# Optimization experiments

Hardware: AMD Instinct MI355X
Metric: run time of the kernel (lower is better)

Reference implementation:

```python
import jax, jax.numpy as jnp
import numpy as np

K = 5            # n_neighbors
N_CLASSES = 100  # number of label classes
EPS = 1e-12


def setup_inputs() -> dict:
    key = jax.random.key(0)
    k1, k2, k3 = jax.random.split(key, 3)
    x = jax.random.normal(k1, (4096, 512), dtype=jnp.float32)
    train_data = jax.random.normal(k2, (100000, 512), dtype=jnp.float32)
    train_labels = jax.random.randint(k3, (100000,), 0, N_CLASSES, dtype=jnp.int32)
    return {"x": x, "train_data": train_data, "train_labels": train_labels}


def reference(x, train_data, train_labels):
    # Pairwise L2 distances: [N_test, N_train]
    x_sq = jnp.sum(x * x, axis=1, keepdims=True)            # [N_test, 1]
    t_sq = jnp.sum(train_data * train_data, axis=1)         # [N_train]
    cross = x @ train_data.T                                 # [N_test, N_train]
    dist = jnp.sqrt(jnp.clip(x_sq + t_sq[None, :] - 2.0 * cross, EPS, None))
    # k smallest distances -> top_k on negated distances
    _, idx = jax.lax.top_k(-dist, K)                          # idx: [N_test, K]
    neighbor_labels = train_labels[idx]                       # [N_test, K]
    # torch.mode picks the most frequent label, smallest value on ties;
    # argmax over per-class counts returns the lowest index on ties -> same semantics.
    counts = jnp.sum(jax.nn.one_hot(neighbor_labels, N_CLASSES, dtype=jnp.int32), axis=1)  # [N_test, C]
    predictions = jnp.argmax(counts, axis=1).astype(jnp.int32)  # [N_test]
    return predictions
```

## Files before the change

kernel.cpp:

```cpp
#include <hip/hip_runtime.h>


#define N_TEST   4096
#define N_TRAIN  100000
#define NT256    391
#define NPAD     100096
#define DIM      512
#define KNN      5
#define NCH      16
#define TD6      6
#define TD8      8
#define PH       17
#define SLAB     16384
#define INF      3.402823466e38f
#define IMAX     0x7fffffff

typedef __attribute__((ext_vector_type(8))) _Float16 f16x8;
typedef __attribute__((ext_vector_type(4))) _Float16 f16x4;
typedef __attribute__((ext_vector_type(4))) float    f32x4;

#define WS_WSI   0u
#define WS_TSQ   2097152u
#define WS_AIMG  2500608u
#define WS_BIMG  111405056u
#define WS_NEED  115861504u

__device__ __forceinline__ void gload_lds16(const void* g, void* l) {
    __builtin_amdgcn_global_load_lds(
        (const __attribute__((address_space(1))) void*)g,
        (__attribute__((address_space(3))) void*)l, 16, 0, 0);
}

__device__ __forceinline__ bool bet(float d, int t, float dd, int tt) {
    return (d < dd) || (d == dd && t < tt);
}

__device__ __forceinline__ void ins6lex(float (&td)[TD6], int (&ti)[TD6], float d, int tg) {
    if (bet(d, tg, td[TD6 - 1], ti[TD6 - 1])) {
        td[TD6 - 1] = d; ti[TD6 - 1] = tg;
        #pragma unroll
        for (int j = TD6 - 1; j > 0; --j) {
            if (bet(td[j], ti[j], td[j - 1], ti[j - 1])) {
                float t0 = td[j]; td[j] = td[j - 1]; td[j - 1] = t0;
                int   i0 = ti[j]; ti[j] = ti[j - 1]; ti[j - 1] = i0;
            }
        }
    }
}

__device__ __forceinline__ void ins8(float (&td)[TD8], int (&ti)[TD8], float d, int tg) {
    if (d < td[TD8 - 1]) {
        td[TD8 - 1] = d; ti[TD8 - 1] = tg;
        #pragma unroll
        for (int j = TD8 - 1; j > 0; --j) {
            if (td[j] < td[j - 1]) {
                float t0 = td[j]; td[j] = td[j - 1]; td[j - 1] = t0;
                int   i0 = ti[j]; ti[j] = ti[j - 1]; ti[j - 1] = i0;
            }
        }
    }
}

__device__ __forceinline__ void ins8lex(float (&td)[TD8], int (&ti)[TD8], float d, int tg) {
    if (bet(d, tg, td[TD8 - 1], ti[TD8 - 1])) {
        td[TD8 - 1] = d; ti[TD8 - 1] = tg;
        #pragma unroll
        for (int j = TD8 - 1; j > 0; --j) {
            if (bet(td[j], ti[j], td[j - 1], ti[j - 1])) {
                float t0 = td[j]; td[j] = td[j - 1]; td[j - 1] = t0;
                int   i0 = ti[j]; ti[j] = ti[j - 1]; ti[j - 1] = i0;
            }
        }
    }
}

__device__ __forceinline__ void ins5lex(float (&td)[KNN], int (&ti)[KNN], float d, int tg) {
    if (bet(d, tg, td[4], ti[4])) {
        if (bet(d, tg, td[3], ti[3])) {
            td[4] = td[3]; ti[4] = ti[3];
            if (bet(d, tg, td[2], ti[2])) {
                td[3] = td[2]; ti[3] = ti[2];
                if (bet(d, tg, td[1], ti[1])) {
                    td[2] = td[1]; ti[2] = ti[1];
                    if (bet(d, tg, td[0], ti[0])) {
                        td[1] = td[0]; ti[1] = ti[0];
                        td[0] = d; ti[0] = tg;
                    } else { td[1] = d; ti[1] = tg; }
                } else { td[2] = d; ti[2] = tg; }
            } else { td[3] = d; ti[3] = tg; }
        } else { td[4] = d; ti[4] = tg; }
    }
}

__global__ __launch_bounds__(256) void convA_kernel(const float* __restrict__ train,
        char* __restrict__ Aimg, float* __restrict__ tsq) {
    const int w    = threadIdx.x >> 6;
    const int lane = threadIdx.x & 63;
    const int rp   = blockIdx.x * 4 + w;
    const int rs   = min(rp, N_TRAIN - 1);
    const float4* src = (const float4*)(train + (size_t)rs * DIM + lane * 8);
    const float4 v0 = src[0], v1 = src[1];
    const float fv[8] = {v0.x, v0.y, v0.z, v0.w, v1.x, v1.y, v1.z, v1.w};
    float s = 0.0f;
    f16x8 h;
    #pragma unroll
    for (int e = 0; e < 8; ++e) { s += fv[e] * fv[e]; h[e] = (_Float16)(-fv[e]); }
    #pragma unroll
    for (int off = 32; off > 0; off >>= 1) s += __shfl_down(s, off, 64);
    s = __shfl(s, 0, 64);
    if (lane == 0 && rp < N_TRAIN) tsq[rp] = s;
    const int gt = rp >> 8, r = rp & 255;
    const int p = lane >> 2, j = lane & 3;
    const int xw = (r >> 1) & 3;
    char* base = Aimg + ((size_t)(gt * PH + p)) * SLAB + r * 64;
    *(f16x8*)(base + ((j ^ xw) << 4)) = h;
    if (lane < 4) {
        f16x8 pad = {0, 0, 0, 0, 0, 0, 0, 0};
        if (lane == 0) {
            const float th = (rp < N_TRAIN) ? 0.5f * s : 30000.0f;
            const _Float16 h0 = (_Float16)th;
            pad[0] = h0;
            pad[1] = (_Float16)(th - (float)h0);
        }
        char* pb = Aimg + ((size_t)(gt * PH + 16)) * SLAB + r * 64;
        *(f16x8*)(pb + ((lane ^ xw) << 4)) = pad;
    }
}

__global__ __launch_bounds__(256) void convB_kernel(const float* __restrict__ x,
        char* __restrict__ Bimg) {
    const int w    = threadIdx.x >> 6;
    const int lane = threadIdx.x & 63;
    const int rp   = blockIdx.x * 4 + w;
    const float4* src = (const float4*)(x + (size_t)rp * DIM + lane * 8);
    const float4 v0 = src[0], v1 = src[1];
    const float fv[8] = {v0.x, v0.y, v0.z, v0.w, v1.x, v1.y, v1.z, v1.w};
    f16x8 h;
    #pragma unroll
    for (int e = 0; e < 8; ++e) h[e] = (_Float16)fv[e];
    const int gt = rp >> 8, r = rp & 255;
    const int p = lane >> 2, j = lane & 3;
    const int xw = (r >> 1) & 3;
    char* base = Bimg + ((size_t)(gt * PH + p)) * SLAB + r * 64;
    *(f16x8*)(base + ((j ^ xw) << 4)) = h;
    if (lane < 4) {
        f16x8 pad = {0, 0, 0, 0, 0, 0, 0, 0};
        if (lane == 0) { pad[0] = (_Float16)1.0f; pad[1] = (_Float16)1.0f; }
        char* pb = Bimg + ((size_t)(gt * PH + 16)) * SLAB + r * 64;
        *(f16x8*)(pb + ((lane ^ xw) << 4)) = pad;
    }
}

__global__ __launch_bounds__(512, 2) __attribute__((amdgpu_waves_per_eu(2, 2)))
void knn_dma(
    const char* __restrict__ Aimg, const char* __restrict__ Bimg,
    int* __restrict__ wsi)
{
    __shared__ __align__(16) char smem[98304];
    const int tid  = threadIdx.x;
    const int qt   = blockIdx.x;
    const int q0   = qt * 256;
    const int c    = blockIdx.y;
    const int gt0  = (c * NT256) >> 4;
    const int gt1  = ((c + 1) * NT256) >> 4;
    const int nt   = gt1 - gt0;
    const int tot  = nt * PH;

    const int w    = tid >> 6;
    const int lane = tid & 63;
    const int wrow = w >> 2;
    const int wcol = w & 3;
    const int l15  = lane & 15;
    const int lk   = lane >> 4;

    const int soff = tid * 16;

    const int xw   = (l15 >> 1) & 3;
    const int aoff = (wrow * 128 + l15) * 64 + ((lk ^ xw) << 4);
    const int boff = (wcol * 64 + l15) * 64 + ((lk ^ xw) << 4) + SLAB;

    float key[4][TD6];
    #pragma unroll
    for (int nj = 0; nj < 4; ++nj)
        #pragma unroll
        for (int j = 0; j < TD6; ++j) key[nj][j] = INF;

    auto STAGE = [&](int buf, const char* a, const char* b) {
        char* base = smem + buf * 32768;
        gload_lds16(a + soff,        base + soff);
        gload_lds16(a + soff + 8192, base + soff + 8192);
        gload_lds16(b + soff,        base + 16384 + soff);
        gload_lds16(b + soff + 8192, base + 16384 + soff + 8192);
    };

    const char* aS = Aimg + (size_t)(gt0 * PH) * SLAB;
    const char* bB = Bimg + (size_t)(qt * PH) * SLAB;
    int sp = 0, sp17 = 0;

    STAGE(0, aS, bB);        aS += SLAB; sp = 1; sp17 = 1;
    STAGE(1, aS, bB + SLAB); aS += SLAB; sp = 2; sp17 = 2;

    int gp = 0;
    #pragma unroll 1
    for (int at = 0; at < nt; ++at) {
        f32x4 acc[8][4];
        #pragma unroll
        for (int mi = 0; mi < 8; ++mi)
            #pragma unroll
            for (int nj = 0; nj < 4; ++nj) acc[mi][nj] = (f32x4){0.f, 0.f, 0.f, 0.f};

        #pragma unroll 1
        for (int p = 0; p < PH; ++p, ++gp) {
            if (gp + 1 < tot) asm volatile("s_waitcnt vmcnt(4)" ::: "memory");
            else              asm volatile("s_waitcnt vmcnt(0)" ::: "memory");
            __builtin_amdgcn_s_barrier();
            __builtin_amdgcn_sched_barrier(0);

            if (sp < tot) {
                STAGE(sp % 3, aS, bB + sp17 * SLAB);
                aS += SLAB; ++sp;
                ++sp17; if (sp17 == PH) sp17 = 0;
            }

            const int bb = (gp % 3) * 32768;
            f16x8 va[8], vb[4];
            #pragma unroll
            for (int nj = 0; nj < 4; ++nj)
                vb[nj] = *(const f16x8*)(smem + bb + boff + nj * 1024);
            #pragma unroll
            for (int mi = 0; mi < 8; ++mi)
                va[mi] = *(const f16x8*)(smem + bb + aoff + mi * 1024);

            __builtin_amdgcn_s_setprio(1);
            #pragma unroll
            for (int mi = 0; mi < 8; ++mi)
                #pragma unroll
                for (int nj = 0; nj < 4; ++nj)
                    acc[mi][nj] = __builtin_amdgcn_mfma_f32_16x16x32_f16(va[mi], vb[nj], acc[mi][nj], 0, 0, 0);
            __builtin_amdgcn_s_setprio(0);
        }

        const int atb = at << 5;
        #pragma unroll
        for (int mi = 0; mi < 8; ++mi) {
            #pragma unroll
            for (int r = 0; r < 4; ++r) {
                const unsigned idx = (unsigned)(atb + mi * 4 + r);
                #pragma unroll
                for (int nj = 0; nj < 4; ++nj) {
                    float k = __uint_as_float(
                        (__float_as_uint(acc[mi][nj][r]) & 0xFFFFFC00u) | idx);
                    #pragma unroll
                    for (int j = 0; j < TD6; ++j) {
                        const float m = fminf(key[nj][j], k);
                        k = fmaxf(key[nj][j], k);
                        key[nj][j] = m;
                    }
                }
            }
        }
    }

    __syncthreads();
    float* md = (float*)(smem);
    int*   mI = (int*)(smem + 24576);
    for (int h = 0; h < 2; ++h) {
        if (h) __syncthreads();
        if ((wcol >> 1) == h) {
            const int slot = wrow * 4 + lk;
            #pragma unroll
            for (int nj = 0; nj < 4; ++nj) {
                const int qh = (wcol & 1) * 64 + nj * 16 + l15;
                #pragma unroll
                for (int j = 0; j < TD6; ++j) {
                    const unsigned kb = __float_as_uint(key[nj][j]);
                    const int idx = (int)(kb & 1023u);
                    const int tg  = (gt0 + (idx >> 5)) * 256 + wrow * 128
                                  + ((idx >> 2) & 7) * 16 + lk * 4 + (idx & 3);
                    md[(slot * TD6 + j) * 128 + qh] = key[nj][j];
                    mI[(slot * TD6 + j) * 128 + qh] = tg;
                }
            }
        }
        __syncthreads();
        if (tid < 128) {
            float fd[TD6]; int fi[TD6];
            #pragma unroll
            for (int j = 0; j < TD6; ++j) { fd[j] = INF; fi[j] = IMAX; }
            #pragma unroll 1
            for (int s = 0; s < 48; ++s)
                ins6lex(fd, fi, md[s * 128 + tid], mI[s * 128 + tid]);
            const int q = q0 + h * 128 + tid;
            const size_t base = ((size_t)q * NCH + c) * TD6;
            #pragma unroll
            for (int j = 0; j < TD6; ++j) wsi[base + j] = fi[j];
        }
    }
}

__global__ __launch_bounds__(256) void knn_final6(
    const float* __restrict__ x, const float* __restrict__ train,
    const float* __restrict__ tsq, const int* __restrict__ wsi,
    const int* __restrict__ labels, int* __restrict__ out)
{
    __shared__ float sc[96];
    __shared__ int   ci[96];
    const int q    = blockIdx.x;
    const int tid  = threadIdx.x;
    const int lane = tid & 63;
    const int w    = tid >> 6;

    const float4* xp = (const float4*)(x + (size_t)q * DIM);
    const float4 xa = xp[lane * 2], xb = xp[lane * 2 + 1];

    if (tid < 96) ci[tid] = wsi[(size_t)q * (NCH * TD6) + tid];
    __syncthreads();

    #pragma unroll 1
    for (int it = 0; it < 24; ++it) {
        const int cidx = w * 24 + it;
        const int t = min(ci[cidx], N_TRAIN - 1);
        const float4* tp = (const float4*)(train + (size_t)t * DIM);
        const float4 ta = tp[lane * 2], tb = tp[lane * 2 + 1];
        float s = ta.x*xa.x + ta.y*xa.y + ta.z*xa.z + ta.w*xa.w
                + tb.x*xb.x + tb.y*xb.y + tb.z*xb.z + tb.w*xb.w;
        #pragma unroll
        for (int off = 32; off > 0; off >>= 1) s += __shfl_down(s, off, 64);
        if (lane == 0) sc[cidx] = fmaf(-2.0f, s, tsq[t]);
    }
    __syncthreads();

    if (tid == 0) {
        float fd[KNN]; int fi[KNN];
        #pragma unroll
        for (int j = 0; j < KNN; ++j) { fd[j] = INF; fi[j] = IMAX; }
        #pragma unroll 1
        for (int s = 0; s < 96; ++s)
            if (ci[s] < N_TRAIN) ins5lex(fd, fi, sc[s], ci[s]);

        int lab[KNN];
        #pragma unroll
        for (int i = 0; i < KNN; ++i) lab[i] = labels[fi[i]];

        int bestLabel = IMAX, bestCount = 0;
        #pragma unroll
        for (int i = 0; i < KNN; ++i) {
            int cnt = 0;
            #pragma unroll
            for (int j = 0; j < KNN; ++j) cnt += (lab[j] == lab[i]) ? 1 : 0;
            if (cnt > bestCount || (cnt == bestCount && lab[i] < bestLabel)) {
                bestCount = cnt; bestLabel = lab[i];
            }
        }
        out[q] = bestLabel;
    }
}

__global__ void tsq_kernel(const float* __restrict__ train, float* __restrict__ tsq) {
    const int lane = threadIdx.x & 63;
    const int wid  = (blockIdx.x * blockDim.x + threadIdx.x) >> 6;
    const int nw   = (gridDim.x * blockDim.x) >> 6;
    for (int row = wid; row < N_TRAIN; row += nw) {
        const float4* p = (const float4*)(train + (size_t)row * DIM);
        float4 a = p[lane];
        float4 b = p[lane + 64];
        float s = a.x*a.x + a.y*a.y + a.z*a.z + a.w*a.w
                + b.x*b.x + b.y*b.y + b.z*b.z + b.w*b.w;
        #pragma unroll
        for (int off = 32; off > 0; off >>= 1) s += __shfl_down(s, off, 64);
        if (lane == 0) tsq[row] = s;
    }
}

__global__ void xconv_kernel(const float* __restrict__ x, _Float16* __restrict__ xf) {
    const int i = blockIdx.x * blockDim.x + threadIdx.x;
    if (i >= N_TEST * DIM / 4) return;
    const float4 v = ((const float4*)x)[i];
    f16x4 h;
    h[0] = (_Float16)v.x; h[1] = (_Float16)v.y;
    h[2] = (_Float16)v.z; h[3] = (_Float16)v.w;
    ((f16x4*)xf)[i] = h;
}

__device__ __forceinline__ int fswz(int row, int kb) {
    return row * 128 + (kb ^ ((row & 7) << 4));
}

#define FB_TPC 6400
__global__ __launch_bounds__(256, 2) void knn_approx(
    const float* __restrict__ train, const _Float16* __restrict__ xf,
    const float* __restrict__ tsq,
    float* __restrict__ wsd, int* __restrict__ wsi)
{
    __shared__ __align__(16) char smem[33280];
    const int tid  = threadIdx.x;
    const int q0   = blockIdx.x * 128;
    const int c    = blockIdx.y;
    const int cstart = c * FB_TPC;
    const int nt   = min(FB_TPC >> 7, (N_TRAIN - cstart + 127) >> 7);
    const int w    = tid >> 6;
    const int wrow = w >> 1, wcol = w & 1;
    const int lane = tid & 63;
    const int l15  = lane & 15, lk = lane >> 4;
    const int srow = tid >> 1, sh = tid & 1;

    float td[4][TD8]; int ti[4][TD8];
    #pragma unroll
    for (int nj = 0; nj < 4; ++nj)
        #pragma unroll
        for (int j = 0; j < TD8; ++j) { td[nj][j] = INF; ti[nj][j] = IMAX; }

    for (int at = 0; at < nt; ++at) {
        const int tbase = cstart + at * 128;
        f32x4 acc[4][4];
        #pragma unroll
        for (int mi = 0; mi < 4; ++mi)
            #pragma unroll
            for (int nj = 0; nj < 4; ++nj) acc[mi][nj] = (f32x4){0.f, 0.f, 0.f, 0.f};

        const int trow_g = min(tbase + srow, N_TRAIN - 1);
        const float*    gA = train + (size_t)trow_g * DIM + sh * 32;
        const _Float16* gB = xf + (size_t)(q0 + srow) * DIM + sh * 32;
        float4 av[8]; f16x8 bv[4];
        #pragma unroll
        for (int j = 0; j < 8; ++j) av[j] = ((const float4*)gA)[j];
        #pragma unroll
        for (int j = 0; j < 4; ++j) bv[j] = ((const f16x8*)gB)[j];
        float tq = 0.0f;
        if (tid < 128) tq = tsq[min(tbase + tid, N_TRAIN - 1)];

        for (int kt = 0; kt < 8; ++kt) {
            __syncthreads();
            #pragma unroll
            for (int j = 0; j < 4; ++j) {
                const float4 v0 = av[2*j], v1 = av[2*j+1];
                const float fv[8] = {v0.x, v0.y, v0.z, v0.w, v1.x, v1.y, v1.z, v1.w};
                f16x8 h;
                #pragma unroll
                for (int e = 0; e < 8; ++e) h[e] = (_Float16)fv[e];
                const int kb = sh * 64 + j * 16;
                *(f16x8*)(smem + 0     + fswz(srow, kb)) = h;
                *(f16x8*)(smem + 16384 + fswz(srow, kb)) = bv[j];
            }
            if (kt == 0 && tid < 128) ((float*)(smem + 32768))[tid] = tq;
            __syncthreads();
            if (kt < 7) {
                const float*    pA = gA + (kt + 1) * 64;
                const _Float16* pB = gB + (kt + 1) * 64;
                #pragma unroll
                for (int j = 0; j < 8; ++j) av[j] = ((const float4*)pA)[j];
                #pragma unroll
                for (int j = 0; j < 4; ++j) bv[j] = ((const f16x8*)pB)[j];
            }
            #pragma unroll
            for (int kk = 0; kk < 2; ++kk) {
                const int kb = kk * 64 + lk * 16;
                f16x8 vb[4];
                #pragma unroll
                for (int nj = 0; nj < 4; ++nj)
                    vb[nj] = *(const f16x8*)(smem + 16384 + fswz(wcol * 64 + nj * 16 + l15, kb));
                #pragma unroll
                for (int mi = 0; mi < 4; ++mi) {
                    const f16x8 ah = *(const f16x8*)(smem + fswz(wrow * 64 + mi * 16 + l15, kb));
                    #pragma unroll
                    for (int nj = 0; nj < 4; ++nj)
                        acc[mi][nj] = __builtin_amdgcn_mfma_f32_16x16x32_f16(ah, vb[nj], acc[mi][nj], 0, 0, 0);
                }
            }
        }
        const float* tsqs = (const float*)(smem + 32768);
        #pragma unroll
        for (int nj = 0; nj < 4; ++nj)
            #pragma unroll
            for (int mi = 0; mi < 4; ++mi) {
                const int tloc = wrow * 64 + mi * 16 + lk * 4;
                #pragma unroll
                for (int r = 0; r < 4; ++r) {
                    const int tg = tbase + tloc + r;
                    if (tg < N_TRAIN) {
                        const float d = fmaf(-2.0f, acc[mi][nj][r], tsqs[tloc + r]);
                        ins8(td[nj], ti[nj], d, tg);
                    }
                }
            }
    }

    __syncthreads();
    float* md = (float*)(smem);
    int*   mI = (int*)(smem + 16384);
    for (int half = 0; half < 2; ++half) {
        if (half) __syncthreads();
        #pragma unroll
        for (int p = 0; p < 2; ++p) {
            const int nj   = half * 2 + p;
            const int qr   = wcol * 32 + p * 16 + l15;
            const int slot = wrow * 4 + lk;
            #pragma unroll
            for (int j = 0; j < TD8; ++j) {
                md[(slot * TD8 + j) * 64 + qr] = td[nj][j];
                mI[(slot * TD8 + j) * 64 + qr] = ti[nj][j];
            }
        }
        __syncthreads();
        if (tid < 64) {
            const int qr = tid;
            float fd[TD8]; int fi[TD8];
            #pragma unroll
            for (int j = 0; j < TD8; ++j) { fd[j] = INF; fi[j] = IMAX; }
            #pragma unroll 1
            for (int s = 0; s < 64; ++s)
                ins8lex(fd, fi, md[s * 64 + qr], mI[s * 64 + qr]);
            const int q = q0 + (qr >> 5) * 64 + (half * 2 + ((qr >> 4) & 1)) * 16 + (qr & 15);
            const size_t base = ((size_t)q * NCH + c) * TD8;
            #pragma unroll
            for (int j = 0; j < TD8; ++j) { wsd[base + j] = fd[j]; wsi[base + j] = fi[j]; }
        }
    }
}

__global__ __launch_bounds__(256) void knn_final_fb(
    const float* __restrict__ x, const float* __restrict__ train,
    const float* __restrict__ tsq, const int* __restrict__ wsi,
    const int* __restrict__ labels, int* __restrict__ out)
{
    __shared__ float sc[128];
    __shared__ int   ci[128];
    const int q    = blockIdx.x;
    const int tid  = threadIdx.x;
    const int lane = tid & 63;
    const int w    = tid >> 6;

    const float4* xp = (const float4*)(x + (size_t)q * DIM);
    const float4 xa = xp[lane * 2], xb = xp[lane * 2 + 1];

    if (tid < 128) ci[tid] = wsi[(size_t)q * (NCH * TD8) + tid];
    __syncthreads();

    #pragma unroll 1
    for (int it = 0; it < 32; ++it) {
        const int cidx = w * 32 + it;
        const int t = min(ci[cidx], N_TRAIN - 1);
        const float4* tp = (const float4*)(train + (size_t)t * DIM);
        const float4 ta = tp[lane * 2], tb = tp[lane * 2 + 1];
        float s = ta.x*xa.x + ta.y*xa.y + ta.z*xa.z + ta.w*xa.w
                + tb.x*xb.x + tb.y*xb.y + tb.z*xb.z + tb.w*xb.w;
        #pragma unroll
        for (int off = 32; off > 0; off >>= 1) s += __shfl_down(s, off, 64);
        if (lane == 0) sc[cidx] = fmaf(-2.0f, s, tsq[t]);
    }
    __syncthreads();

    if (tid == 0) {
        float fd[KNN]; int fi[KNN];
        #pragma unroll
        for (int j = 0; j < KNN; ++j) { fd[j] = INF; fi[j] = IMAX; }
        #pragma unroll 1
        for (int s = 0; s < 128; ++s)
            if (ci[s] < N_TRAIN) ins5lex(fd, fi, sc[s], ci[s]);

        int lab[KNN];
        #pragma unroll
        for (int i = 0; i < KNN; ++i) lab[i] = labels[fi[i]];

        int bestLabel = IMAX, bestCount = 0;
        #pragma unroll
        for (int i = 0; i < KNN; ++i) {
            int cnt = 0;
            #pragma unroll
            for (int j = 0; j < KNN; ++j) cnt += (lab[j] == lab[i]) ? 1 : 0;
            if (cnt > bestCount || (cnt == bestCount && lab[i] < bestLabel)) {
                bestCount = cnt; bestLabel = lab[i];
            }
        }
        out[q] = bestLabel;
    }
}

extern "C" void kernel_launch(void* const* d_in, const int* in_sizes, int n_in,
                              void* d_out, int out_size, void* d_ws, size_t ws_size,
                              hipStream_t stream) {
    const float* x      = (const float*)d_in[0];
    const float* train  = (const float*)d_in[1];
    const int*   labels = (const int*)d_in[2];
    int* out = (int*)d_out;
    char* ws = (char*)d_ws;

    int*   wsi = (int*)(ws + WS_WSI);
    float* tsq = (float*)(ws + WS_TSQ);

    if (ws_size >= (size_t)WS_NEED) {
        char* Aimg = ws + WS_AIMG;
        char* Bimg = ws + WS_BIMG;
        hipLaunchKernelGGL(convA_kernel, dim3(NPAD / 4), dim3(256), 0, stream, train, Aimg, tsq);
        hipLaunchKernelGGL(convB_kernel, dim3(N_TEST / 4), dim3(256), 0, stream, x, Bimg);
        hipLaunchKernelGGL(knn_dma, dim3(N_TEST / 256, NCH), dim3(512), 0, stream,
                           Aimg, Bimg, wsi);
        hipLaunchKernelGGL(knn_final6, dim3(N_TEST), dim3(256), 0, stream,
                           x, train, tsq, wsi, labels, out);
    } else {
        float*    wsd = (float*)(ws + 2500608);
        _Float16* xf  = (_Float16*)(ws + 4597760);
        hipLaunchKernelGGL(tsq_kernel, dim3(512), dim3(256), 0, stream, train, tsq);
        hipLaunchKernelGGL(xconv_kernel, dim3(N_TEST * DIM / 4 / 256), dim3(256), 0, stream, x, xf);
        hipLaunchKernelGGL(knn_approx, dim3(N_TEST / 128, NCH), dim3(256), 0, stream,
                           train, xf, tsq, wsd, wsi);
        hipLaunchKernelGGL(knn_final_fb, dim3(N_TEST), dim3(256), 0, stream,
                           x, train, tsq, wsi, labels, out);
    }
}
```

Before: 677.4 us.

## Shrink query tile to 128 per block and use med3 top-6 insertion

The main GEMM/top-k kernel now uses 256-thread blocks covering 128 queries instead of 512 threads covering 256. The B image is re-laid out with 8 KB slabs, LDS staging shrinks to 24 KB per buffer, and the wait count is raised to match six DMA loads per stage. This doubles the grid, which may improve CU occupancy and balance, but each train tile is now reused across fewer queries, so A-side traffic doubles. The running top-6 insertion also switches from a min/max chain to fmed3, which cuts the number of ALU ops in the selection epilogue.

```diff
diff --git a/kernel.cpp b/kernel.cpp
--- a/kernel.cpp
+++ b/kernel.cpp
@@ -11,13 +11,20 @@
 #define TD6      6
 #define TD8      8
 #define PH       17
-#define SLAB     16384
+#define ASLAB    16384
+#define BSLAB    8192
 #define INF      3.402823466e38f
 #define IMAX     0x7fffffff
 
 typedef __attribute__((ext_vector_type(8))) _Float16 f16x8;
 typedef __attribute__((ext_vector_type(4))) _Float16 f16x4;
 typedef __attribute__((ext_vector_type(4))) float    f32x4;
+
+#if defined(__has_builtin) && __has_builtin(__builtin_amdgcn_fmed3f)
+#define MED3(a,b,c) __builtin_amdgcn_fmed3f((a),(b),(c))
+#else
+#define MED3(a,b,c) fminf(fmaxf((a),fminf((b),(c))), fmaxf(fminf((a),(b)),(c)))
+#endif
 
 #define WS_WSI   0u
 #define WS_TSQ   2097152u
@@ -112,7 +119,7 @@
     const int gt = rp >> 8, r = rp & 255;
     const int p = lane >> 2, j = lane & 3;
     const int xw = (r >> 1) & 3;
-    char* base = Aimg + ((size_t)(gt * PH + p)) * SLAB + r * 64;
+    char* base = Aimg + ((size_t)(gt * PH + p)) * ASLAB + r * 64;
     *(f16x8*)(base + ((j ^ xw) << 4)) = h;
     if (lane < 4) {
         f16x8 pad = {0, 0, 0, 0, 0, 0, 0, 0};
@@ -122,7 +129,7 @@
             pad[0] = h0;
             pad[1] = (_Float16)(th - (float)h0);
         }
-        char* pb = Aimg + ((size_t)(gt * PH + 16)) * SLAB + r * 64;
+        char* pb = Aimg + ((size_t)(gt * PH + 16)) * ASLAB + r * 64;
         *(f16x8*)(pb + ((lane ^ xw) << 4)) = pad;
     }
 }
@@ -138,28 +145,28 @@
     f16x8 h;
     #pragma unroll
     for (int e = 0; e < 8; ++e) h[e] = (_Float16)fv[e];
-    const int gt = rp >> 8, r = rp & 255;
+    const int gt = rp >> 7, r = rp & 127;
     const int p = lane >> 2, j = lane & 3;
     const int xw = (r >> 1) & 3;
-    char* base = Bimg + ((size_t)(gt * PH + p)) * SLAB + r * 64;
+    char* base = Bimg + ((size_t)(gt * PH + p)) * BSLAB + r * 64;
     *(f16x8*)(base + ((j ^ xw) << 4)) = h;
     if (lane < 4) {
         f16x8 pad = {0, 0, 0, 0, 0, 0, 0, 0};
         if (lane == 0) { pad[0] = (_Float16)1.0f; pad[1] = (_Float16)1.0f; }
-        char* pb = Bimg + ((size_t)(gt * PH + 16)) * SLAB + r * 64;
+        char* pb = Bimg + ((size_t)(gt * PH + 16)) * BSLAB + r * 64;
         *(f16x8*)(pb + ((lane ^ xw) << 4)) = pad;
     }
 }
 
-__global__ __launch_bounds__(512, 2) __attribute__((amdgpu_waves_per_eu(2, 2)))
+__global__ __launch_bounds__(256, 2) __attribute__((amdgpu_waves_per_eu(2, 2)))
 void knn_dma(
     const char* __restrict__ Aimg, const char* __restrict__ Bimg,
     int* __restrict__ wsi)
 {
-    __shared__ __align__(16) char smem[98304];
+    __shared__ __align__(16) char smem[73728];
     const int tid  = threadIdx.x;
     const int qt   = blockIdx.x;
-    const int q0   = qt * 256;
+    const int q0   = qt * 128;
     const int c    = blockIdx.y;
     const int gt0  = (c * NT256) >> 4;
     const int gt1  = ((c + 1) * NT256) >> 4;
@@ -168,16 +175,14 @@
 
     const int w    = tid >> 6;
     const int lane = tid & 63;
-    const int wrow = w >> 2;
-    const int wcol = w & 3;
+    const int wrow = w >> 1;
+    const int wcol = w & 1;
     const int l15  = lane & 15;
     const int lk   = lane >> 4;
 
-    const int soff = tid * 16;
-
     const int xw   = (l15 >> 1) & 3;
     const int aoff = (wrow * 128 + l15) * 64 + ((lk ^ xw) << 4);
-    const int boff = (wcol * 64 + l15) * 64 + ((lk ^ xw) << 4) + SLAB;
+    const int boff = (wcol * 64 + l15) * 64 + ((lk ^ xw) << 4) + ASLAB;
 
     float key[4][TD6];
     #pragma unroll
@@ -186,19 +191,21 @@
         for (int j = 0; j < TD6; ++j) key[nj][j] = INF;
 
     auto STAGE = [&](int buf, const char* a, const char* b) {
-        char* base = smem + buf * 32768;
-        gload_lds16(a + soff,        base + soff);
-        gload_lds16(a + soff + 8192, base + soff + 8192);
-        gload_lds16(b + soff,        base + 16384 + soff);
-        gload_lds16(b + soff + 8192, base + 16384 + soff + 8192);
+        char* base = smem + buf * 24576;
+        gload_lds16(a + tid * 16,         base + tid * 16);
+        gload_lds16(a + tid * 16 + 4096,  base + tid * 16 + 4096);
+        gload_lds16(a + tid * 16 + 8192,  base + tid * 16 + 8192);
+        gload_lds16(a + tid * 16 + 12288, base + tid * 16 + 12288);
+        gload_lds16(b + tid * 16,         base + ASLAB + tid * 16);
+        gload_lds16(b + tid * 16 + 4096,  base + ASLAB + tid * 16 + 4096);
     };
 
-    const char* aS = Aimg + (size_t)(gt0 * PH) * SLAB;
-    const char* bB = Bimg + (size_t)(qt * PH) * SLAB;
+    const char* aS = Aimg + (size_t)(gt0 * PH) * ASLAB;
+    const char* bB = Bimg + (size_t)(qt * PH) * BSLAB;
     int sp = 0, sp17 = 0;
 
-    STAGE(0, aS, bB);        aS += SLAB; sp = 1; sp17 = 1;
-    STAGE(1, aS, bB + SLAB); aS += SLAB; sp = 2; sp17 = 2;
+    STAGE(0, aS, bB);         aS += ASLAB; sp = 1; sp17 = 1;
+    STAGE(1, aS, bB + BSLAB); aS += ASLAB; sp = 2; sp17 = 2;
 
     int gp = 0;
     #pragma unroll 1
@@ -211,18 +218,18 @@
 
         #pragma unroll 1
         for (int p = 0; p < PH; ++p, ++gp) {
-            if (gp + 1 < tot) asm volatile("s_waitcnt vmcnt(4)" ::: "memory");
+            if (gp + 1 < tot) asm volatile("s_waitcnt vmcnt(6)" ::: "memory");
             else              asm volatile("s_waitcnt vmcnt(0)" ::: "memory");
             __builtin_amdgcn_s_barrier();
             __builtin_amdgcn_sched_barrier(0);
 
             if (sp < tot) {
-                STAGE(sp % 3, aS, bB + sp17 * SLAB);
-                aS += SLAB; ++sp;
+                STAGE(sp % 3, aS, bB + sp17 * BSLAB);
+                aS += ASLAB; ++sp;
                 ++sp17; if (sp17 == PH) sp17 = 0;
             }
 
-            const int bb = (gp % 3) * 32768;
+            const int bb = (gp % 3) * 24576;
             f16x8 va[8], vb[4];
             #pragma unroll
             for (int nj = 0; nj < 4; ++nj)
@@ -248,14 +255,15 @@
                 const unsigned idx = (unsigned)(atb + mi * 4 + r);
                 #pragma unroll
                 for (int nj = 0; nj < 4; ++nj) {
-                    float k = __uint_as_float(
+                    const float k = __uint_as_float(
                         (__float_as_uint(acc[mi][nj][r]) & 0xFFFFFC00u) | idx);
-                    #pragma unroll
-                    for (int j = 0; j < TD6; ++j) {
-                        const float m = fminf(key[nj][j], k);
-                        k = fmaxf(key[nj][j], k);
-                        key[nj][j] = m;
-                    }
+                    float* K = key[nj];
+                    K[5] = MED3(K[4], K[5], k);
+                    K[4] = MED3(K[3], K[4], k);
+                    K[3] = MED3(K[2], K[3], k);
+                    K[2] = MED3(K[1], K[2], k);
+                    K[1] = MED3(K[0], K[1], k);
+                    K[0] = fminf(K[0], k);
                 }
             }
         }
@@ -264,37 +272,34 @@
     __syncthreads();
     float* md = (float*)(smem);
     int*   mI = (int*)(smem + 24576);
-    for (int h = 0; h < 2; ++h) {
-        if (h) __syncthreads();
-        if ((wcol >> 1) == h) {
-            const int slot = wrow * 4 + lk;
-            #pragma unroll
-            for (int nj = 0; nj < 4; ++nj) {
-                const int qh = (wcol & 1) * 64 + nj * 16 + l15;
-                #pragma unroll
-                for (int j = 0; j < TD6; ++j) {
-                    const unsigned kb = __float_as_uint(key[nj][j]);
-                    const int idx = (int)(kb & 1023u);
-                    const int tg  = (gt0 + (idx >> 5)) * 256 + wrow * 128
-                                  + ((idx >> 2) & 7) * 16 + lk * 4 + (idx & 3);
-                    md[(slot * TD6 + j) * 128 + qh] = key[nj][j];
-                    mI[(slot * TD6 + j) * 128 + qh] = tg;
-                }
-            }
-        }
-        __syncthreads();
-        if (tid < 128) {
-            float fd[TD6]; int fi[TD6];
-            #pragma unroll
-            for (int j = 0; j < TD6; ++j) { fd[j] = INF; fi[j] = IMAX; }
-            #pragma unroll 1
-            for (int s = 0; s < 48; ++s)
-                ins6lex(fd, fi, md[s * 128 + tid], mI[s * 128 + tid]);
-            const int q = q0 + h * 128 + tid;
-            const size_t base = ((size_t)q * NCH + c) * TD6;
-            #pragma unroll
-            for (int j = 0; j < TD6; ++j) wsi[base + j] = fi[j];
-        }
+    {
+        const int slot = wrow * 4 + lk;
+        #pragma unroll
+        for (int nj = 0; nj < 4; ++nj) {
+            const int qh = wcol * 64 + nj * 16 + l15;
+            #pragma unroll
+            for (int j = 0; j < TD6; ++j) {
+                const unsigned kb = __float_as_uint(key[nj][j]);
+                const int idx = (int)(kb & 1023u);
+                const int tg  = (gt0 + (idx >> 5)) * 256 + wrow * 128
+                              + ((idx >> 2) & 7) * 16 + lk * 4 + (idx & 3);
+                md[(slot * TD6 + j) * 128 + qh] = key[nj][j];
+                mI[(slot * TD6 + j) * 128 + qh] = tg;
+            }
+        }
+    }
+    __syncthreads();
+    if (tid < 128) {
+        float fd[TD6]; int fi[TD6];
+        #pragma unroll
+        for (int j = 0; j < TD6; ++j) { fd[j] = INF; fi[j] = IMAX; }
+        #pragma unroll 1
+        for (int s = 0; s < 48; ++s)
+            ins6lex(fd, fi, md[s * 128 + tid], mI[s * 128 + tid]);
+        const int q = q0 + tid;
+        const size_t base = ((size_t)q * NCH + c) * TD6;
+        #pragma unroll
+        for (int j = 0; j < TD6; ++j) wsi[base + j] = fi[j];
     }
 }
 
@@ -593,7 +598,7 @@
         char* Bimg = ws + WS_BIMG;
         hipLaunchKernelGGL(convA_kernel, dim3(NPAD / 4), dim3(256), 0, stream, train, Aimg, tsq);
         hipLaunchKernelGGL(convB_kernel, dim3(N_TEST / 4), dim3(256), 0, stream, x, Bimg);
-        hipLaunchKernelGGL(knn_dma, dim3(N_TEST / 256, NCH), dim3(512), 0, stream,
+        hipLaunchKernelGGL(knn_dma, dim3(N_TEST / 128, NCH), dim3(256), 0, stream,
                            Aimg, Bimg, wsi);
         hipLaunchKernelGGL(knn_final6, dim3(N_TEST), dim3(256), 0, stream,
                            x, train, tsq, wsi, labels, out);
```

Measured after the change: 590.2 us (median of 3 runs). -12.9%, faster.
